# Kernel tuning notes

Measured on AMD Instinct MI355X. Metric: run time of the kernel, lower is better.

Reference implementation:

```python
import jax, jax.numpy as jnp
import numpy as np

B, S, D = 4, 2048, 1024
H = 4 * D          # expert hidden dim
E_SPEC = 4         # num specific experts
E_SHR = 2          # num shared experts
TOP_K = 2


def setup_inputs() -> dict:
    key = jax.random.key(0)
    ks = jax.random.split(key, 16)
    s = 0.02
    return {
        "x": jax.random.normal(ks[0], (B, S, D), jnp.float32),
        # specific experts (stacked over expert axis)
        "spec_w1": jax.random.normal(ks[1], (E_SPEC, D, H), jnp.float32) * s,
        "spec_b1": jnp.zeros((E_SPEC, H), jnp.float32),
        "spec_w2": jax.random.normal(ks[2], (E_SPEC, H, D), jnp.float32) * s,
        "spec_b2": jnp.zeros((E_SPEC, D), jnp.float32),
        "spec_rw": jax.random.normal(ks[3], (D, E_SPEC), jnp.float32) * s,
        "spec_rb": jnp.zeros((E_SPEC,), jnp.float32),
        # shared experts
        "shr_w1": jax.random.normal(ks[4], (E_SHR, D, H), jnp.float32) * s,
        "shr_b1": jnp.zeros((E_SHR, H), jnp.float32),
        "shr_w2": jax.random.normal(ks[5], (E_SHR, H, D), jnp.float32) * s,
        "shr_b2": jnp.zeros((E_SHR, D), jnp.float32),
        "shr_rw": jax.random.normal(ks[6], (D, E_SHR), jnp.float32) * s,
        "shr_rb": jnp.zeros((E_SHR,), jnp.float32),
    }


def _expert_mlp(xf, w1, b1, w2, b2):
    # xf: [T, D]; w1: [E, D, H]; w2: [E, H, D] -> [E, T, D]
    h = jax.nn.gelu(jnp.einsum("td,edh->eth", xf, w1) + b1[:, None, :],
                    approximate=False)
    return jnp.einsum("eth,ehd->etd", h, w2) + b2[:, None, :]


def reference(x, spec_w1, spec_b1, spec_w2, spec_b2, spec_rw, spec_rb,
              shr_w1, shr_b1, shr_w2, shr_b2, shr_rw, shr_rb):
    b, s, d = x.shape
    xf = x.reshape(-1, d)                      # [T, D]
    T = xf.shape[0]

    # --- specific (top-k) routing ---
    spec_probs = jax.nn.softmax(xf @ spec_rw + spec_rb, axis=-1)   # [T, E]
    topk_probs, topk_idx = jax.lax.top_k(spec_probs, TOP_K)        # [T, K]

    # aux load-balancing loss
    counts = jnp.zeros((E_SPEC,), jnp.float32).at[topk_idx.reshape(-1)].add(1.0)
    fraction = counts / (T * TOP_K)
    aux_loss = E_SPEC * jnp.sum(fraction * spec_probs.mean(axis=0))

    # gate[t, e] = sum_k topk_probs[t,k] * 1[topk_idx[t,k]==e]
    gate = jnp.sum(jax.nn.one_hot(topk_idx, E_SPEC, dtype=xf.dtype)
                   * topk_probs[..., None], axis=1)                # [T, E]

    spec_out_e = _expert_mlp(xf, spec_w1, spec_b1, spec_w2, spec_b2)  # [E, T, D]
    specific_out = jnp.einsum("te,etd->td", gate, spec_out_e)

    # --- shared (dense) experts ---
    shr_probs = jax.nn.softmax(xf @ shr_rw + shr_rb, axis=-1)      # [T, E_shr]
    shr_out_e = _expert_mlp(xf, shr_w1, shr_b1, shr_w2, shr_b2)    # [E_shr, T, D]
    shared_out = jnp.einsum("te,etd->td", shr_probs, shr_out_e)

    final = (specific_out + shared_out).reshape(b, s, d)
    return final, aux_loss
```

## Files before the change

kernel.cpp:

```cpp
#include <hip/hip_runtime.h>
#include <hip/hip_bf16.h>

#define T_TOK 8192
#define DDIM 1024
#define HDIM 4096

typedef __bf16 bf16;
typedef bf16 bf16x8 __attribute__((ext_vector_type(8)));
typedef float f32x4 __attribute__((ext_vector_type(4)));

#define ASM_VMCNT(n) asm volatile("s_waitcnt vmcnt(" #n ")" ::: "memory")
#define MFMA16(a, b, c) __builtin_amdgcn_mfma_f32_16x16x32_bf16((a), (b), (c), 0, 0, 0)
#define G8_BAR __builtin_amdgcn_s_barrier()
#define G8_WAIT                                            \
  asm volatile("s_waitcnt lgkmcnt(0)" ::: "memory");       \
  __builtin_amdgcn_sched_barrier(0)

__device__ __forceinline__ void gl_lds16(const void* g, void* l) {
  __builtin_amdgcn_global_load_lds(
      (const __attribute__((address_space(1))) unsigned int*)g,
      (__attribute__((address_space(3))) unsigned int*)l, 16, 0, 0);
}

__device__ __forceinline__ float gelu_f(float v) {
  const float x = v * 0.7071067811865475f;
  const float ax = fabsf(x);
  const float t = 1.0f / fmaf(0.3275911f, ax, 1.0f);
  float p = fmaf(1.061405429f, t, -1.453152027f);
  p = fmaf(p, t, 1.421413741f);
  p = fmaf(p, t, -0.284496736f);
  p = fmaf(p, t, 0.254829592f);
  p = p * t;
  const float e = __expf(-ax * ax);
  const float er = fmaf(-p, e, 1.0f);
  const float erfx = (x >= 0.0f) ? er : -er;
  return 0.5f * v * (1.0f + erfx);
}

__global__ __launch_bounds__(256) void conv_router(
    const float* __restrict__ x, bf16* __restrict__ xb,
    const float* __restrict__ srw, const float* __restrict__ srb,
    const float* __restrict__ hrw, const float* __restrict__ hrb,
    float* __restrict__ gate, float4* __restrict__ probs4,
    int* __restrict__ top2) {
  const int lane = threadIdx.x & 63;
  const int w = threadIdx.x >> 6;
  const int t = blockIdx.x * 4 + w;

  const float* xr = x + (size_t)t * DDIM;
  bf16* xbr = xb + (size_t)t * DDIM;
  float p0 = 0, p1 = 0, p2 = 0, p3 = 0, p4 = 0, p5 = 0;
#pragma unroll
  for (int c = 0; c < 4; ++c) {
    const int d = c * 256 + lane * 4;
    const float4 xv = *(const float4*)(xr + d);
    bf16 ov[4] = {(bf16)xv.x, (bf16)xv.y, (bf16)xv.z, (bf16)xv.w};
    *(float2*)(xbr + d) = *(float2*)ov;
    const float xa[4] = {xv.x, xv.y, xv.z, xv.w};
#pragma unroll
    for (int j = 0; j < 4; ++j) {
      const float xd = xa[j];
      const float4 r4 = *(const float4*)(srw + (size_t)(d + j) * 4);
      p0 += xd * r4.x; p1 += xd * r4.y; p2 += xd * r4.z; p3 += xd * r4.w;
      const float2 r2 = *(const float2*)(hrw + (size_t)(d + j) * 2);
      p4 += xd * r2.x; p5 += xd * r2.y;
    }
  }
#pragma unroll
  for (int off = 32; off >= 1; off >>= 1) {
    p0 += __shfl_xor(p0, off);
    p1 += __shfl_xor(p1, off);
    p2 += __shfl_xor(p2, off);
    p3 += __shfl_xor(p3, off);
    p4 += __shfl_xor(p4, off);
    p5 += __shfl_xor(p5, off);
  }
  if (lane == 0) {
    const float l0 = p0 + srb[0], l1 = p1 + srb[1];
    const float l2 = p2 + srb[2], l3 = p3 + srb[3];
    const float m = fmaxf(fmaxf(l0, l1), fmaxf(l2, l3));
    const float e0 = expf(l0 - m), e1 = expf(l1 - m);
    const float e2 = expf(l2 - m), e3 = expf(l3 - m);
    const float s = e0 + e1 + e2 + e3;
    float pr[4] = {e0 / s, e1 / s, e2 / s, e3 / s};
    int i1 = 0; float v1 = pr[0];
#pragma unroll
    for (int e = 1; e < 4; ++e) if (pr[e] > v1) { v1 = pr[e]; i1 = e; }
    int i2 = -1; float v2 = -1.0f;
#pragma unroll
    for (int e = 0; e < 4; ++e)
      if (e != i1 && pr[e] > v2) { v2 = pr[e]; i2 = e; }
    float g[4] = {0, 0, 0, 0};
    g[i1] = v1; g[i2] = v2;
    float* gr = gate + (size_t)t * 8;
    gr[0] = g[0]; gr[1] = g[1]; gr[2] = g[2]; gr[3] = g[3];
    const float h0 = p4 + hrb[0], h1 = p5 + hrb[1];
    const float mh = fmaxf(h0, h1);
    const float q0 = expf(h0 - mh), q1 = expf(h1 - mh);
    const float qs = q0 + q1;
    gr[4] = q0 / qs; gr[5] = q1 / qs; gr[6] = 0; gr[7] = 0;
    probs4[t] = make_float4(pr[0], pr[1], pr[2], pr[3]);
    top2[t] = i1 | (i2 << 8);
  }
}

__global__ __launch_bounds__(256) void transpose_convert6(
    const float* __restrict__ spec_w, const float* __restrict__ shr_w,
    bf16* __restrict__ dst, int R, int C) {
  __shared__ float tile[32][33];
  const int z = blockIdx.z;
  const float* src = (z < 4) ? spec_w + (size_t)z * R * C
                             : shr_w + (size_t)(z - 4) * R * C;
  bf16* d = dst + (size_t)z * R * C;
  const int c0 = blockIdx.x * 32, r0 = blockIdx.y * 32;
  const int tx = threadIdx.x & 31, ty = threadIdx.x >> 5;
#pragma unroll
  for (int i = 0; i < 4; ++i)
    tile[ty + 8 * i][tx] = src[(size_t)(r0 + ty + 8 * i) * C + c0 + tx];
  __syncthreads();
#pragma unroll
  for (int i = 0; i < 4; ++i)
    d[(size_t)(c0 + ty + 8 * i) * R + r0 + tx] = (bf16)tile[tx][ty + 8 * i];
}

__global__ __launch_bounds__(1024) void scan_build(
    const int* __restrict__ top2, const float4* __restrict__ probs4,
    int* __restrict__ meta, int* __restrict__ lists,
    float* __restrict__ auxg) {
  __shared__ unsigned long long sc[1024];
  __shared__ float4 rp[512];
  const int tid = threadIdx.x;

  int ee[8];
  unsigned long long c = 0;
  float4 ps = make_float4(0.f, 0.f, 0.f, 0.f);
#pragma unroll
  for (int j = 0; j < 8; ++j) {
    const int t = tid * 8 + j;
    const int p = top2[t];
    ee[j] = p;
    const int a = p & 15, b = (p >> 8) & 15;
    c += (1ULL << (16 * a)) + (1ULL << (16 * b));
    const float4 pv = probs4[t];
    ps.x += pv.x; ps.y += pv.y; ps.z += pv.z; ps.w += pv.w;
  }
  sc[tid] = c;
  __syncthreads();
  for (int off = 1; off < 1024; off <<= 1) {
    const unsigned long long mine = sc[tid];
    const unsigned long long prev = (tid >= off) ? sc[tid - off] : 0ULL;
    __syncthreads();
    sc[tid] = mine + prev;
    __syncthreads();
  }
  const unsigned long long incl = sc[tid];
  const unsigned long long tot = sc[1023];
  const unsigned long long excl = incl - c;
  int q0 = (int)(excl & 0xffff), q1 = (int)((excl >> 16) & 0xffff);
  int q2 = (int)((excl >> 32) & 0xffff), q3 = (int)((excl >> 48) & 0xffff);
#pragma unroll
  for (int j = 0; j < 8; ++j) {
    const int t = tid * 8 + j;
    const int a = ee[j] & 15, b = (ee[j] >> 8) & 15;
    const int pa = (a == 0) ? q0 : (a == 1) ? q1 : (a == 2) ? q2 : q3;
    lists[a * 8192 + pa] = t;
    q0 += (a == 0); q1 += (a == 1); q2 += (a == 2); q3 += (a == 3);
    const int pb = (b == 0) ? q0 : (b == 1) ? q1 : (b == 2) ? q2 : q3;
    lists[b * 8192 + pb] = t;
    q0 += (b == 0); q1 += (b == 1); q2 += (b == 2); q3 += (b == 3);
  }
  if (tid == 1023) {
    const int c0 = (int)(tot & 0xffff), c1 = (int)((tot >> 16) & 0xffff);
    const int c2 = (int)((tot >> 32) & 0xffff), c3 = (int)((tot >> 48) & 0xffff);
    meta[24] = c0; meta[25] = c1; meta[26] = c2; meta[27] = c3;
    auxg[0] = (float)c0; auxg[1] = (float)c1;
    auxg[2] = (float)c2; auxg[3] = (float)c3;
    const int nb0 = (c0 + 255) >> 8, nb1 = (c1 + 255) >> 8;
    const int nb2 = (c2 + 255) >> 8, nb3 = (c3 + 255) >> 8;
    const int ch0 = (nb0 + 3) >> 2, ch1 = (nb1 + 3) >> 2;
    const int ch2 = (nb2 + 3) >> 2, ch3 = (nb3 + 3) >> 2;
    meta[34] = 0;
    meta[35] = nb0 * 256;
    meta[36] = meta[35] + nb1 * 256;
    meta[37] = meta[36] + nb2 * 256;
    meta[40] = 0;
    meta[41] = 64 * ch0;
    meta[42] = meta[41] + 64 * ch1;
    meta[43] = meta[42] + 64 * ch2;
    meta[44] = meta[43] + 64 * ch3;
  }
  if (tid >= 512) rp[tid - 512] = ps;
  __syncthreads();
  if (tid < 512) {
    const float4 o = rp[tid];
    ps.x += o.x; ps.y += o.y; ps.z += o.z; ps.w += o.w;
  }
  for (int w = 256; w >= 1; w >>= 1) {
    __syncthreads();
    if (tid >= w && tid < 2 * w) rp[tid - w] = ps;
    __syncthreads();
    if (tid < w) {
      const float4 o = rp[tid];
      ps.x += o.x; ps.y += o.y; ps.z += o.z; ps.w += o.w;
    }
  }
  if (tid == 0) {
    auxg[4] = ps.x; auxg[5] = ps.y; auxg[6] = ps.z; auxg[7] = ps.w;
  }
}

__global__ void aux_finalize(const float* __restrict__ auxg,
                             float* __restrict__ outp) {
  float a = 0.0f;
#pragma unroll
  for (int e = 0; e < 4; ++e)
    a += (auxg[e] / (float)(T_TOK * 2)) * (auxg[4 + e] / (float)T_TOK);
  outp[0] = 4.0f * a;
}

template <int KIND>
__global__ __launch_bounds__(512, 2) void g8(
    const bf16* __restrict__ A, const bf16* __restrict__ Bw,
    const float* __restrict__ bias, bf16* __restrict__ h_all, int N,
    int CH_M, int CH_N, const int* __restrict__ meta,
    const int* __restrict__ lists, int e) {
  __shared__ __align__(1024) bf16 Alds[2 * 256 * 64];
  __shared__ __align__(1024) bf16 Blds[2 * 256 * 64];

  const int tid = threadIdx.x;
  const int lane = tid & 63, wid = tid >> 6;
  const int wm = wid >> 2, wn = wid & 3;
  const int lr = lane & 15, lg = lane >> 4;

  int bm, bn, hb = 0, s = e;
  const bf16* Bp = Bw;
  const float* biasp = bias;
  if constexpr (KIND == 0) {
    const int xcd = blockIdx.x & 7, idx = blockIdx.x >> 3;
    bm = (xcd >> 1) * CH_M + idx / CH_N;
    bn = (xcd & 1) * CH_N + idx % CH_N;
  } else if constexpr (KIND == 1) {
    const int b = blockIdx.x;
    if (b >= meta[44]) return;
    s = (b >= meta[41]) + (b >= meta[42]) + (b >= meta[43]);
    const int local = b - meta[40 + s];
    const int nbm = (meta[24 + s] + 255) >> 8;
    const int CHm = (nbm + 3) >> 2;
    if (local >= 64 * CHm) return;
    const int xc = local & 7, idx = local >> 3;
    bm = (xc >> 1) * CHm + idx / 8;
    bn = (xc & 1) * 8 + idx % 8;
    if (bm >= nbm) return;
    hb = meta[34 + s];
    Bp = Bw + (size_t)s * DDIM * HDIM;
    biasp = bias + (size_t)s * HDIM;
  } else {
    const int nbm = (meta[24 + e] + 255) >> 8;
    const int CHm = (nbm + 3) >> 2;
    if (blockIdx.x >= 64 * CHm) return;
    const int xc = blockIdx.x & 7, idx = blockIdx.x >> 3;
    bm = (xc >> 1) * CHm + idx / 8;
    bn = (xc & 1) * 8 + idx % 8;
    if (bm >= nbm) return;
  }
  const int K = DDIM;
  const int NT = K >> 6;

  const int rl = tid >> 3;
  const int cbs = ((tid * 16) & 127) ^ ((rl & 7) << 4);
  int ar[4];
#pragma unroll
  for (int c = 0; c < 4; ++c) ar[c] = bm * 256 + c * 64 + rl;
  if constexpr (KIND != 0) {
    const int* lp = lists + s * 8192;
#pragma unroll
    for (int c = 0; c < 4; ++c) {
      const int t = lp[ar[c]];
      ar[c] = t < 0 ? 0 : t;
    }
  }
  const bf16* sA[4];
  const bf16* sB[4];
#pragma unroll
  for (int c = 0; c < 4; ++c) {
    sA[c] = A + (size_t)ar[c] * K + (cbs >> 1);
    sB[c] = Bp + (size_t)(bn * 256 + c * 64 + rl) * K + (cbs >> 1);
  }
  char* const ldsA = (char*)Alds;
  char* const ldsB = (char*)Blds;
  const int wb = wid * 1024;

  const int ax0 = (lg * 16) ^ ((lr & 7) << 4);
  const int ax1 = ax0 ^ 64;
  const int aro = (wm * 128 + lr) * 128;
  const int bro = (wn * 64 + lr) * 128;
  const char* const A0 = (const char*)Alds + aro + ax0;
  const char* const A1 = (const char*)Alds + aro + ax1;
  const char* const B0 = (const char*)Blds + bro + ax0;
  const char* const B1 = (const char*)Blds + bro + ax1;

  f32x4 acc[8][4] = {};
  bf16x8 af[4][2], b01[2][2], b23[2][2];

#define G8_RA(BOFF, MB)                                               \
  _Pragma("unroll") for (int i = 0; i < 4; ++i) {                     \
    af[i][0] = *(const bf16x8*)(A0 + (BOFF) + ((MB) + i) * 2048);     \
    af[i][1] = *(const bf16x8*)(A1 + (BOFF) + ((MB) + i) * 2048);     \
  }
#define G8_RB(BOFF, DST, NB)                                          \
  _Pragma("unroll") for (int i = 0; i < 2; ++i) {                     \
    DST[i][0] = *(const bf16x8*)(B0 + (BOFF) + ((NB) + i) * 2048);    \
    DST[i][1] = *(const bf16x8*)(B1 + (BOFF) + ((NB) + i) * 2048);    \
  }
#define G8_MMA(MB, NB, BSRC)                                          \
  __builtin_amdgcn_s_setprio(1);                                      \
  _Pragma("unroll") for (int i = 0; i < 4; ++i)                       \
    _Pragma("unroll") for (int j = 0; j < 2; ++j) {                   \
      acc[(MB) + i][(NB) + j] =                                       \
          MFMA16(af[i][0], BSRC[j][0], acc[(MB) + i][(NB) + j]);      \
      acc[(MB) + i][(NB) + j] =                                       \
          MFMA16(af[i][1], BSRC[j][1], acc[(MB) + i][(NB) + j]);      \
    }                                                                 \
  __builtin_amdgcn_s_setprio(0);
#define G8_STG_B(T, C, BUFO)                                          \
  gl_lds16(sB[C] + (size_t)(T) * 64, ldsB + (BUFO) + (C) * 8192 + wb);
#define G8_STG_A(T, C, BUFO)                                          \
  gl_lds16(sA[C] + (size_t)(T) * 64, ldsA + (BUFO) + (C) * 8192 + wb);

  G8_STG_B(0, 0, 0) G8_STG_B(0, 1, 0) G8_STG_B(0, 2, 0) G8_STG_B(0, 3, 0)
  G8_STG_A(0, 0, 0) G8_STG_A(0, 1, 0) G8_STG_A(0, 2, 0) G8_STG_A(0, 3, 0)
  G8_STG_B(1, 0, 32768) G8_STG_B(1, 1, 32768)
  G8_STG_B(1, 2, 32768) G8_STG_B(1, 3, 32768)
  G8_STG_A(1, 0, 32768) G8_STG_A(1, 1, 32768)
  G8_STG_A(1, 2, 32768) G8_STG_A(1, 3, 32768)
  ASM_VMCNT(8);
  G8_BAR;

  for (int t = 0; t < NT; t += 2) {
    const bool stg = (t + 2) < NT;
    G8_RA(0, 0);
    G8_RB(0, b01, 0);
    G8_BAR; G8_WAIT;
    G8_MMA(0, 0, b01);
    G8_BAR;
    G8_RB(0, b23, 2);
    G8_BAR; G8_WAIT;
    G8_MMA(0, 2, b23);
    G8_BAR;
    G8_RA(0, 4);
    if (stg) { G8_STG_B(t + 2, 0, 0) G8_STG_B(t + 2, 1, 0) }
    G8_BAR; G8_WAIT;
    G8_MMA(4, 0, b01);
    G8_BAR;
    if (stg) { G8_STG_B(t + 2, 2, 0) G8_STG_B(t + 2, 3, 0) }
    G8_MMA(4, 2, b23);
    if (stg) ASM_VMCNT(4); else ASM_VMCNT(0);
    G8_BAR;
    G8_RA(32768, 0);
    G8_RB(32768, b01, 0);
    if (stg) { G8_STG_A(t + 2, 0, 0) G8_STG_A(t + 2, 1, 0) }
    G8_BAR; G8_WAIT;
    G8_MMA(0, 0, b01);
    G8_BAR;
    G8_RB(32768, b23, 2);
    if (stg) { G8_STG_A(t + 2, 2, 0) G8_STG_A(t + 2, 3, 0) }
    G8_BAR; G8_WAIT;
    G8_MMA(0, 2, b23);
    G8_BAR;
    G8_RA(32768, 4);
    if (stg) {
      G8_STG_B(t + 3, 0, 32768) G8_STG_B(t + 3, 1, 32768)
      G8_STG_B(t + 3, 2, 32768) G8_STG_B(t + 3, 3, 32768)
    }
    G8_BAR; G8_WAIT;
    G8_MMA(4, 0, b01);
    G8_BAR;
    if (stg) {
      G8_STG_A(t + 3, 0, 32768) G8_STG_A(t + 3, 1, 32768)
      G8_STG_A(t + 3, 2, 32768) G8_STG_A(t + 3, 3, 32768)
    }
    G8_MMA(4, 2, b23);
    if (stg) ASM_VMCNT(8);
    G8_BAR;
  }

  const int colb = bn * 256 + wn * 64;
  const int rowb = hb + bm * 256 + wm * 128 + lg * 4;
  float bv[4];
#pragma unroll
  for (int nf = 0; nf < 4; ++nf) bv[nf] = biasp[colb + nf * 16 + lr];
#pragma unroll
  for (int mf = 0; mf < 8; ++mf)
#pragma unroll
    for (int nf = 0; nf < 4; ++nf) {
      const int col = colb + nf * 16 + lr;
#pragma unroll
      for (int r = 0; r < 4; ++r) {
        const int row = rowb + mf * 16 + r;
        h_all[(size_t)row * N + col] = (bf16)gelu_f(acc[mf][nf][r] + bv[nf]);
      }
    }
}

template <int EMODE>
__global__ __launch_bounds__(512, 2) void g2k(
    const bf16* __restrict__ A, int lda, const bf16* __restrict__ B,
    const float* __restrict__ bias, float* __restrict__ out,
    const float* __restrict__ gate, int gidx, const int* __restrict__ meta,
    const int* __restrict__ lists, int e, int packed) {
  __shared__ __align__(1024) bf16 Alds[2 * 256 * 64];
  __shared__ __align__(1024) bf16 Blds[2 * 128 * 64];

  const int tid = threadIdx.x;
  const int lane = tid & 63, wid = tid >> 6;
  const int wm = wid >> 2, wn = wid & 3;
  const int lr = lane & 15, lg = lane >> 4;

  int bm, bn, hb = 0;
  if constexpr (EMODE == 3) {
    const int nbm = (meta[24 + e] + 255) >> 8;
    const int CHm = (nbm + 3) >> 2;
    if (blockIdx.x >= 8 * CHm * 4) return;
    const int xc = blockIdx.x & 7, idx = blockIdx.x >> 3;
    bm = (xc >> 1) * CHm + idx / 4;
    bn = (xc & 1) * 4 + idx % 4;
    if (bm >= nbm) return;
    hb = packed ? meta[34 + e] : 0;
  } else {
    const int xcd = blockIdx.x & 7, idx = blockIdx.x >> 3;
    bm = (xcd >> 1) * 8 + idx / 4;
    bn = (xcd & 1) * 4 + idx % 4;
  }
  const int K = HDIM, N = DDIM;
  const int NT = K >> 6;

  const int L = tid * 16;
  const int rl = L >> 7;
  const int colb = (L & 127) ^ ((rl & 7) << 4);

  const int ar0 = hb + bm * 256 + rl;
  const bf16* sAc0 = A + (size_t)ar0 * lda + (colb >> 1);
  const bf16* sAc1 = A + (size_t)(ar0 + 64) * lda + (colb >> 1);
  const bf16* sAc2 = A + (size_t)(ar0 + 128) * lda + (colb >> 1);
  const bf16* sAc3 = A + (size_t)(ar0 + 192) * lda + (colb >> 1);
  const bf16* sB = B + (size_t)(bn * 128 + rl) * K + (colb >> 1);

  char* const ldsA = (char*)Alds;
  char* const ldsB = (char*)Blds;
  const int wb = wid * 1024;
  char* const stA[2] = {ldsA + wb, ldsA + 32768 + wb};
  char* const stB[2] = {ldsB + wb, ldsB + 16384 + wb};

  const int ax0 = (lg * 16) ^ ((lr & 7) << 4);
  const int ax1 = ax0 ^ 64;
  const int aro = (wm * 128 + lr) * 128;
  const int bro = (wn * 32 + lr) * 128;
  const char* const Ak0[2] = {ldsA + aro + ax0, ldsA + 32768 + aro + ax0};
  const char* const Ak1[2] = {ldsA + aro + ax1, ldsA + 32768 + aro + ax1};
  const char* const Bk0[2] = {ldsB + bro + ax0, ldsB + 16384 + bro + ax0};
  const char* const Bk1[2] = {ldsB + bro + ax1, ldsB + 16384 + bro + ax1};

  f32x4 acc[8][2] = {};

  gl_lds16(sAc0, stA[0]);
  gl_lds16(sAc1, stA[0] + 8192);
  gl_lds16(sAc2, stA[0] + 16384);
  gl_lds16(sAc3, stA[0] + 24576);
  gl_lds16(sB, stB[0]);
  gl_lds16(sB + (size_t)64 * K, stB[0] + 8192);
  gl_lds16(sB + 64, stB[1]);
  gl_lds16(sB + (size_t)64 * K + 64, stB[1] + 8192);
  gl_lds16(sAc0 + 64, stA[1]);
  gl_lds16(sAc1 + 64, stA[1] + 8192);
  ASM_VMCNT(4);
  __builtin_amdgcn_s_barrier();

  for (int kt0 = 0; kt0 < NT; kt0 += 2) {
#pragma unroll
    for (int par = 0; par < 2; ++par) {
      const int kt = kt0 + par;
      const int cur = par, oth = par ^ 1;
      const bool st1 = (kt + 1) < NT, st2 = (kt + 2) < NT;
      const size_t ko1 = (size_t)(kt + 1) << 6, ko2 = (size_t)(kt + 2) << 6;
      const char* Ac0 = Ak0[cur]; const char* Ac1 = Ak1[cur];
      const char* Bc0 = Bk0[cur]; const char* Bc1 = Bk1[cur];

      bf16x8 af[4][2], bfr[2][2];

#pragma unroll
      for (int mf = 0; mf < 4; ++mf) {
        af[mf][0] = *(const bf16x8*)(Ac0 + mf * 2048);
        af[mf][1] = *(const bf16x8*)(Ac1 + mf * 2048);
      }
      bfr[0][0] = *(const bf16x8*)(Bc0);
      bfr[0][1] = *(const bf16x8*)(Bc1);
      if (st1) {
        gl_lds16(sAc2 + ko1, stA[oth] + 16384);
        gl_lds16(sAc3 + ko1, stA[oth] + 24576);
      }
      __builtin_amdgcn_s_barrier();
      asm volatile("s_waitcnt lgkmcnt(0)" ::: "memory");
      __builtin_amdgcn_sched_barrier(0);
      __builtin_amdgcn_s_setprio(1);
#pragma unroll
      for (int mf = 0; mf < 4; ++mf) {
        acc[mf][0] = MFMA16(af[mf][0], bfr[0][0], acc[mf][0]);
        acc[mf][0] = MFMA16(af[mf][1], bfr[0][1], acc[mf][0]);
      }
      __builtin_amdgcn_s_setprio(0);
      __builtin_amdgcn_s_barrier();

      bfr[1][0] = *(const bf16x8*)(Bc0 + 2048);
      bfr[1][1] = *(const bf16x8*)(Bc1 + 2048);
      __builtin_amdgcn_s_barrier();
      asm volatile("s_waitcnt lgkmcnt(0)" ::: "memory");
      __builtin_amdgcn_sched_barrier(0);
      __builtin_amdgcn_s_setprio(1);
#pragma unroll
      for (int mf = 0; mf < 4; ++mf) {
        acc[mf][1] = MFMA16(af[mf][0], bfr[1][0], acc[mf][1]);
        acc[mf][1] = MFMA16(af[mf][1], bfr[1][1], acc[mf][1]);
      }
      __builtin_amdgcn_s_setprio(0);
      __builtin_amdgcn_s_barrier();

#pragma unroll
      for (int mf = 0; mf < 4; ++mf) {
        af[mf][0] = *(const bf16x8*)(Ac0 + 8192 + mf * 2048);
        af[mf][1] = *(const bf16x8*)(Ac1 + 8192 + mf * 2048);
      }
      if (st2) {
        gl_lds16(sB + ko2, stB[cur]);
        gl_lds16(sB + (size_t)64 * K + ko2, stB[cur] + 8192);
      }
      __builtin_amdgcn_s_barrier();
      asm volatile("s_waitcnt lgkmcnt(0)" ::: "memory");
      __builtin_amdgcn_sched_barrier(0);
      __builtin_amdgcn_s_setprio(1);
#pragma unroll
      for (int mf = 0; mf < 4; ++mf) {
        acc[4 + mf][0] = MFMA16(af[mf][0], bfr[0][0], acc[4 + mf][0]);
        acc[4 + mf][0] = MFMA16(af[mf][1], bfr[0][1], acc[4 + mf][0]);
      }
      __builtin_amdgcn_s_setprio(0);
      __builtin_amdgcn_s_barrier();

      if (st2) {
        gl_lds16(sAc0 + ko2, stA[cur]);
        gl_lds16(sAc1 + ko2, stA[cur] + 8192);
      }
      __builtin_amdgcn_s_setprio(1);
#pragma unroll
      for (int mf = 0; mf < 4; ++mf) {
        acc[4 + mf][1] = MFMA16(af[mf][0], bfr[1][0], acc[4 + mf][1]);
        acc[4 + mf][1] = MFMA16(af[mf][1], bfr[1][1], acc[4 + mf][1]);
      }
      __builtin_amdgcn_s_setprio(0);
      if (st2) {
        ASM_VMCNT(4);
        __builtin_amdgcn_s_barrier();
      } else if (st1) {
        ASM_VMCNT(0);
        __builtin_amdgcn_s_barrier();
      }
    }
  }

  const int colb2 = bn * 128 + wn * 32;
  const int rowb = bm * 256 + wm * 128 + lg * 4;
  float bv[2];
#pragma unroll
  for (int nf = 0; nf < 2; ++nf) bv[nf] = bias[colb2 + nf * 16 + lr];
#pragma unroll
  for (int mf = 0; mf < 8; ++mf) {
    if constexpr (EMODE != 3) {
      float gv[4];
#pragma unroll
      for (int r = 0; r < 4; ++r)
        gv[r] = gate[(size_t)(rowb + mf * 16 + r) * 8 + gidx];
#pragma unroll
      for (int nf = 0; nf < 2; ++nf) {
        const int col = colb2 + nf * 16 + lr;
#pragma unroll
        for (int r = 0; r < 4; ++r) {
          const float v = acc[mf][nf][r] + bv[nf];
          const size_t oi = (size_t)(rowb + mf * 16 + r) * N + col;
          if constexpr (EMODE == 1)
            out[oi] += gv[r] * v;
          else
            out[oi] = gv[r] * v;
        }
      }
    } else {
      const int* lp = lists + e * 8192;
      int tok[4]; float gv[4];
#pragma unroll
      for (int r = 0; r < 4; ++r) {
        tok[r] = lp[rowb + mf * 16 + r];
        gv[r] = tok[r] >= 0 ? gate[(size_t)tok[r] * 8 + gidx] : 0.0f;
      }
#pragma unroll
      for (int nf = 0; nf < 2; ++nf) {
        const int col = colb2 + nf * 16 + lr;
#pragma unroll
        for (int r = 0; r < 4; ++r) {
          if (tok[r] >= 0) {
            const float v = acc[mf][nf][r] + bv[nf];
            out[(size_t)tok[r] * N + col] += gv[r] * v;
          }
        }
      }
    }
  }
}

extern "C" void kernel_launch(void* const* d_in, const int* in_sizes, int n_in,
                              void* d_out, int out_size, void* d_ws,
                              size_t ws_size, hipStream_t stream) {
  const float* x = (const float*)d_in[0];
  const float* spec_w1 = (const float*)d_in[1];
  const float* spec_b1 = (const float*)d_in[2];
  const float* spec_w2 = (const float*)d_in[3];
  const float* spec_b2 = (const float*)d_in[4];
  const float* spec_rw = (const float*)d_in[5];
  const float* spec_rb = (const float*)d_in[6];
  const float* shr_w1 = (const float*)d_in[7];
  const float* shr_b1 = (const float*)d_in[8];
  const float* shr_w2 = (const float*)d_in[9];
  const float* shr_b2 = (const float*)d_in[10];
  const float* shr_rw = (const float*)d_in[11];
  const float* shr_rb = (const float*)d_in[12];
  float* out = (float*)d_out;

  char* ws = (char*)d_ws;
  const size_t DH = (size_t)DDIM * HDIM;
  const size_t OFF_W1 = 16777216;
  const size_t OFF_W2 = OFF_W1 + 50331648;
  const size_t OFF_GATE = OFF_W2 + 50331648;
  const size_t OFF_AUX = OFF_GATE + 262144;
  const size_t OFF_META = OFF_AUX + 256;
  const size_t OFF_LIST = OFF_META + 256;
  const size_t OFF_T2 = OFF_LIST + 131072;
  const size_t OFF_P4 = OFF_T2 + 32768;
  const size_t OFF_H = OFF_P4 + 131072 + 1024;
  bf16* xb = (bf16*)ws;
  bf16* w1t = (bf16*)(ws + OFF_W1);
  bf16* w2t = (bf16*)(ws + OFF_W2);
  float* gate = (float*)(ws + OFF_GATE);
  float* auxg = (float*)(ws + OFF_AUX);
  int* meta = (int*)(ws + OFF_META);
  int* lists = (int*)(ws + OFF_LIST);
  int* top2 = (int*)(ws + OFF_T2);
  float4* probs4 = (float4*)(ws + OFF_P4);
  bf16* h = (bf16*)(ws + OFF_H);

  const bool rich = ws_size >= OFF_H + (size_t)17408 * HDIM * 2;

  hipMemsetAsync(lists, 0xFF, 4 * 8192 * 4, stream);

  conv_router<<<T_TOK / 4, 256, 0, stream>>>(x, xb, spec_rw, spec_rb, shr_rw,
                                             shr_rb, gate, probs4, top2);
  scan_build<<<1, 1024, 0, stream>>>(top2, probs4, meta, lists, auxg);

  transpose_convert6<<<dim3(HDIM / 32, DDIM / 32, 6), 256, 0, stream>>>(
      spec_w1, shr_w1, w1t, DDIM, HDIM);
  transpose_convert6<<<dim3(DDIM / 32, HDIM / 32, 6), 256, 0, stream>>>(
      spec_w2, shr_w2, w2t, HDIM, DDIM);

  if (rich) {
    g8<0><<<1024, 512, 0, stream>>>(xb, w1t + 4 * DH, shr_b1, h, 8192,
                                    8, 16, meta, lists, 0);
    g2k<0><<<256, 512, 0, stream>>>(h, 8192, w2t + 4 * DH, shr_b2, out,
                                    gate, 4, meta, lists, 0, 0);
    g2k<1><<<256, 512, 0, stream>>>(h + 4096, 8192, w2t + 5 * DH,
                                    shr_b2 + 1024, out, gate, 5, meta,
                                    lists, 0, 0);
    g8<1><<<2048, 512, 0, stream>>>(xb, w1t, spec_b1, h, 4096,
                                    0, 8, meta, lists, 0);
    for (int e = 0; e < 4; ++e)
      g2k<3><<<256, 512, 0, stream>>>(h, 4096, w2t + (size_t)e * DH,
                                      spec_b2 + (size_t)e * DDIM, out, gate,
                                      e, meta, lists, e, 1);
  } else {
    for (int es = 0; es < 2; ++es) {
      g8<0><<<512, 512, 0, stream>>>(xb, w1t + (4 + es) * DH,
                                     shr_b1 + (size_t)es * HDIM, h, 4096,
                                     8, 8, meta, lists, 0);
      if (es == 0)
        g2k<0><<<256, 512, 0, stream>>>(h, 4096, w2t + 4 * DH, shr_b2, out,
                                        gate, 4, meta, lists, 0, 0);
      else
        g2k<1><<<256, 512, 0, stream>>>(h, 4096, w2t + 5 * DH,
                                        shr_b2 + 1024, out, gate, 5, meta,
                                        lists, 0, 0);
    }
    for (int e = 0; e < 4; ++e) {
      g8<2><<<512, 512, 0, stream>>>(xb, w1t + (size_t)e * DH,
                                     spec_b1 + (size_t)e * HDIM, h, 4096,
                                     0, 8, meta, lists, e);
      g2k<3><<<256, 512, 0, stream>>>(h, 4096, w2t + (size_t)e * DH,
                                      spec_b2 + (size_t)e * DDIM, out, gate,
                                      e, meta, lists, e, 0);
    }
  }
  aux_finalize<<<1, 1, 0, stream>>>(auxg, out + (size_t)T_TOK * DDIM);
}
```

Before: 1.016 ms.

## Batch specific-expert down-projection into one grouped GEMM with gather reduce

Replaces the four per-expert down-projection launches, which scattered gated results into the output with read-modify-write, with a single grouped GEMM over all experts' packed hidden rows. That GEMM writes gated bf16 partials into a scratch buffer that reuses the w1 workspace. A new per-token reduce kernel then gathers each token's two partials via recorded list positions and adds them to the output. This removes the scattered atomic-free RMW traffic and the extra launches, at the cost of a bf16 intermediate round trip and reduced precision of the partials. It also drops the fallback path for small workspaces.

```diff
diff --git a/kernel.cpp b/kernel.cpp
--- a/kernel.cpp
+++ b/kernel.cpp
@@ -125,7 +125,7 @@
 
 __global__ __launch_bounds__(1024) void scan_build(
     const int* __restrict__ top2, const float4* __restrict__ probs4,
-    int* __restrict__ meta, int* __restrict__ lists,
+    int* __restrict__ meta, int* __restrict__ lists, int2* __restrict__ tpos,
     float* __restrict__ auxg) {
   __shared__ unsigned long long sc[1024];
   __shared__ float4 rp[512];
@@ -168,6 +168,7 @@
     const int pb = (b == 0) ? q0 : (b == 1) ? q1 : (b == 2) ? q2 : q3;
     lists[b * 8192 + pb] = t;
     q0 += (b == 0); q1 += (b == 1); q2 += (b == 2); q3 += (b == 3);
+    tpos[t] = make_int2(a * 8192 + pa, b * 8192 + pb);
   }
   if (tid == 1023) {
     const int c0 = (int)(tot & 0xffff), c1 = (int)((tot >> 16) & 0xffff);
@@ -188,6 +189,11 @@
     meta[42] = meta[41] + 64 * ch1;
     meta[43] = meta[42] + 64 * ch2;
     meta[44] = meta[43] + 64 * ch3;
+    meta[52] = 0;
+    meta[53] = 16 * ch0;
+    meta[54] = meta[53] + 16 * ch1;
+    meta[55] = meta[54] + 16 * ch2;
+    meta[56] = meta[55] + 16 * ch3;
   }
   if (tid >= 512) rp[tid - 512] = ps;
   __syncthreads();
@@ -221,9 +227,9 @@
 template <int KIND>
 __global__ __launch_bounds__(512, 2) void g8(
     const bf16* __restrict__ A, const bf16* __restrict__ Bw,
-    const float* __restrict__ bias, bf16* __restrict__ h_all, int N,
+    const float* __restrict__ bias, bf16* __restrict__ Out, int N,
     int CH_M, int CH_N, const int* __restrict__ meta,
-    const int* __restrict__ lists, int e) {
+    const int* __restrict__ lists, const float* __restrict__ gate) {
   __shared__ __align__(1024) bf16 Alds[2 * 256 * 64];
   __shared__ __align__(1024) bf16 Blds[2 * 256 * 64];
 
@@ -232,7 +238,7 @@
   const int wm = wid >> 2, wn = wid & 3;
   const int lr = lane & 15, lg = lane >> 4;
 
-  int bm, bn, hb = 0, s = e;
+  int bm, bn, hb = 0, s = 0;
   const bf16* Bp = Bw;
   const float* biasp = bias;
   if constexpr (KIND == 0) {
@@ -255,29 +261,39 @@
     Bp = Bw + (size_t)s * DDIM * HDIM;
     biasp = bias + (size_t)s * HDIM;
   } else {
-    const int nbm = (meta[24 + e] + 255) >> 8;
+    const int b = blockIdx.x;
+    if (b >= meta[56]) return;
+    s = (b >= meta[53]) + (b >= meta[54]) + (b >= meta[55]);
+    const int local = b - meta[52 + s];
+    const int nbm = (meta[24 + s] + 255) >> 8;
     const int CHm = (nbm + 3) >> 2;
-    if (blockIdx.x >= 64 * CHm) return;
-    const int xc = blockIdx.x & 7, idx = blockIdx.x >> 3;
-    bm = (xc >> 1) * CHm + idx / 8;
-    bn = (xc & 1) * 8 + idx % 8;
+    if (local >= 16 * CHm) return;
+    const int xc = local & 7, idx = local >> 3;
+    bm = (xc >> 1) * CHm + idx / 2;
+    bn = (xc & 1) * 2 + idx % 2;
     if (bm >= nbm) return;
-  }
-  const int K = DDIM;
-  const int NT = K >> 6;
+    hb = meta[34 + s];
+    Bp = Bw + (size_t)s * DDIM * HDIM;
+    biasp = bias + (size_t)s * DDIM;
+  }
+  constexpr int K = (KIND == 2) ? HDIM : DDIM;
+  constexpr int NT = K >> 6;
 
   const int rl = tid >> 3;
   const int cbs = ((tid * 16) & 127) ^ ((rl & 7) << 4);
   int ar[4];
 #pragma unroll
   for (int c = 0; c < 4; ++c) ar[c] = bm * 256 + c * 64 + rl;
-  if constexpr (KIND != 0) {
+  if constexpr (KIND == 1) {
     const int* lp = lists + s * 8192;
 #pragma unroll
     for (int c = 0; c < 4; ++c) {
       const int t = lp[ar[c]];
       ar[c] = t < 0 ? 0 : t;
     }
+  } else if constexpr (KIND == 2) {
+#pragma unroll
+    for (int c = 0; c < 4; ++c) ar[c] += hb;
   }
   const bf16* sA[4];
   const bf16* sB[4];
@@ -385,29 +401,53 @@
   }
 
   const int colb = bn * 256 + wn * 64;
-  const int rowb = hb + bm * 256 + wm * 128 + lg * 4;
-  float bv[4];
-#pragma unroll
-  for (int nf = 0; nf < 4; ++nf) bv[nf] = biasp[colb + nf * 16 + lr];
-#pragma unroll
-  for (int mf = 0; mf < 8; ++mf)
-#pragma unroll
-    for (int nf = 0; nf < 4; ++nf) {
-      const int col = colb + nf * 16 + lr;
+  const int lrowb = bm * 256 + wm * 128 + lg * 4;
+  if constexpr (KIND != 2) {
+    float bv[4];
+#pragma unroll
+    for (int nf = 0; nf < 4; ++nf) bv[nf] = biasp[colb + nf * 16 + lr];
+#pragma unroll
+    for (int mf = 0; mf < 8; ++mf)
+#pragma unroll
+      for (int nf = 0; nf < 4; ++nf) {
+        const int col = colb + nf * 16 + lr;
+#pragma unroll
+        for (int r = 0; r < 4; ++r) {
+          const int row = hb + lrowb + mf * 16 + r;
+          Out[(size_t)row * N + col] = (bf16)gelu_f(acc[mf][nf][r] + bv[nf]);
+        }
+      }
+  } else {
+    float bv[4];
+#pragma unroll
+    for (int nf = 0; nf < 4; ++nf) bv[nf] = biasp[colb + nf * 16 + lr];
+    const int* lp = lists + s * 8192;
+#pragma unroll
+    for (int mf = 0; mf < 8; ++mf) {
+      int tok[4]; float gv[4];
 #pragma unroll
       for (int r = 0; r < 4; ++r) {
-        const int row = rowb + mf * 16 + r;
-        h_all[(size_t)row * N + col] = (bf16)gelu_f(acc[mf][nf][r] + bv[nf]);
+        tok[r] = lp[lrowb + mf * 16 + r];
+        gv[r] = tok[r] >= 0 ? gate[(size_t)tok[r] * 8 + s] : 0.0f;
+      }
+#pragma unroll
+      for (int nf = 0; nf < 4; ++nf) {
+        const int col = colb + nf * 16 + lr;
+#pragma unroll
+        for (int r = 0; r < 4; ++r) {
+          const float v = gv[r] * (acc[mf][nf][r] + bv[nf]);
+          Out[(size_t)(hb + lrowb + mf * 16 + r) * N + col] = (bf16)v;
+        }
       }
     }
+  }
 }
 
 template <int EMODE>
 __global__ __launch_bounds__(512, 2) void g2k(
     const bf16* __restrict__ A, int lda, const bf16* __restrict__ B,
     const float* __restrict__ bias, float* __restrict__ out,
-    const float* __restrict__ gate, int gidx, const int* __restrict__ meta,
-    const int* __restrict__ lists, int e, int packed) {
+    const float* __restrict__ gate, int gidx) {
   __shared__ __align__(1024) bf16 Alds[2 * 256 * 64];
   __shared__ __align__(1024) bf16 Blds[2 * 128 * 64];
 
@@ -416,21 +456,9 @@
   const int wm = wid >> 2, wn = wid & 3;
   const int lr = lane & 15, lg = lane >> 4;
 
-  int bm, bn, hb = 0;
-  if constexpr (EMODE == 3) {
-    const int nbm = (meta[24 + e] + 255) >> 8;
-    const int CHm = (nbm + 3) >> 2;
-    if (blockIdx.x >= 8 * CHm * 4) return;
-    const int xc = blockIdx.x & 7, idx = blockIdx.x >> 3;
-    bm = (xc >> 1) * CHm + idx / 4;
-    bn = (xc & 1) * 4 + idx % 4;
-    if (bm >= nbm) return;
-    hb = packed ? meta[34 + e] : 0;
-  } else {
-    const int xcd = blockIdx.x & 7, idx = blockIdx.x >> 3;
-    bm = (xcd >> 1) * 8 + idx / 4;
-    bn = (xcd & 1) * 4 + idx % 4;
-  }
+  const int xcd = blockIdx.x & 7, idx = blockIdx.x >> 3;
+  const int bm = (xcd >> 1) * 8 + idx / 4;
+  const int bn = (xcd & 1) * 4 + idx % 4;
   const int K = HDIM, N = DDIM;
   const int NT = K >> 6;
 
@@ -438,7 +466,7 @@
   const int rl = L >> 7;
   const int colb = (L & 127) ^ ((rl & 7) << 4);
 
-  const int ar0 = hb + bm * 256 + rl;
+  const int ar0 = bm * 256 + rl;
   const bf16* sAc0 = A + (size_t)ar0 * lda + (colb >> 1);
   const bf16* sAc1 = A + (size_t)(ar0 + 64) * lda + (colb >> 1);
   const bf16* sAc2 = A + (size_t)(ar0 + 128) * lda + (colb >> 1);
@@ -573,45 +601,42 @@
   for (int nf = 0; nf < 2; ++nf) bv[nf] = bias[colb2 + nf * 16 + lr];
 #pragma unroll
   for (int mf = 0; mf < 8; ++mf) {
-    if constexpr (EMODE != 3) {
-      float gv[4];
-#pragma unroll
-      for (int r = 0; r < 4; ++r)
-        gv[r] = gate[(size_t)(rowb + mf * 16 + r) * 8 + gidx];
-#pragma unroll
-      for (int nf = 0; nf < 2; ++nf) {
-        const int col = colb2 + nf * 16 + lr;
-#pragma unroll
-        for (int r = 0; r < 4; ++r) {
-          const float v = acc[mf][nf][r] + bv[nf];
-          const size_t oi = (size_t)(rowb + mf * 16 + r) * N + col;
-          if constexpr (EMODE == 1)
-            out[oi] += gv[r] * v;
-          else
-            out[oi] = gv[r] * v;
-        }
-      }
-    } else {
-      const int* lp = lists + e * 8192;
-      int tok[4]; float gv[4];
+    float gv[4];
+#pragma unroll
+    for (int r = 0; r < 4; ++r)
+      gv[r] = gate[(size_t)(rowb + mf * 16 + r) * 8 + gidx];
+#pragma unroll
+    for (int nf = 0; nf < 2; ++nf) {
+      const int col = colb2 + nf * 16 + lr;
 #pragma unroll
       for (int r = 0; r < 4; ++r) {
-        tok[r] = lp[rowb + mf * 16 + r];
-        gv[r] = tok[r] >= 0 ? gate[(size_t)tok[r] * 8 + gidx] : 0.0f;
-      }
-#pragma unroll
-      for (int nf = 0; nf < 2; ++nf) {
-        const int col = colb2 + nf * 16 + lr;
-#pragma unroll
-        for (int r = 0; r < 4; ++r) {
-          if (tok[r] >= 0) {
-            const float v = acc[mf][nf][r] + bv[nf];
-            out[(size_t)tok[r] * N + col] += gv[r] * v;
-          }
-        }
+        const float v = acc[mf][nf][r] + bv[nf];
+        const size_t oi = (size_t)(rowb + mf * 16 + r) * N + col;
+        if constexpr (EMODE == 1)
+          out[oi] += gv[r] * v;
+        else
+          out[oi] = gv[r] * v;
       }
     }
   }
+}
+
+__global__ __launch_bounds__(256) void reduce_spec(
+    const bf16* __restrict__ P, const int2* __restrict__ tpos,
+    const int* __restrict__ meta, float* __restrict__ out) {
+  const int t = blockIdx.x;
+  const int c = threadIdx.x * 4;
+  const int2 tp = tpos[t];
+  const int ea = tp.x >> 13, pa = tp.x & 8191;
+  const int eb = tp.y >> 13, pb = tp.y & 8191;
+  const bf16* A4 = &P[(size_t)(meta[34 + ea] + pa) * DDIM + c];
+  const bf16* B4 = &P[(size_t)(meta[34 + eb] + pb) * DDIM + c];
+  float4 o = *(float4*)&out[(size_t)t * DDIM + c];
+  o.x += (float)A4[0] + (float)B4[0];
+  o.y += (float)A4[1] + (float)B4[1];
+  o.z += (float)A4[2] + (float)B4[2];
+  o.w += (float)A4[3] + (float)B4[3];
+  *(float4*)&out[(size_t)t * DDIM + c] = o;
 }
 
 extern "C" void kernel_launch(void* const* d_in, const int* in_sizes, int n_in,
@@ -642,7 +667,8 @@
   const size_t OFF_LIST = OFF_META + 256;
   const size_t OFF_T2 = OFF_LIST + 131072;
   const size_t OFF_P4 = OFF_T2 + 32768;
-  const size_t OFF_H = OFF_P4 + 131072 + 1024;
+  const size_t OFF_TPOS = OFF_P4 + 131072 + 1024;
+  const size_t OFF_H = OFF_TPOS + 65536;
   bf16* xb = (bf16*)ws;
   bf16* w1t = (bf16*)(ws + OFF_W1);
   bf16* w2t = (bf16*)(ws + OFF_W2);
@@ -652,56 +678,32 @@
   int* lists = (int*)(ws + OFF_LIST);
   int* top2 = (int*)(ws + OFF_T2);
   float4* probs4 = (float4*)(ws + OFF_P4);
+  int2* tpos = (int2*)(ws + OFF_TPOS);
   bf16* h = (bf16*)(ws + OFF_H);
-
-  const bool rich = ws_size >= OFF_H + (size_t)17408 * HDIM * 2;
+  bf16* P = w1t;
 
   hipMemsetAsync(lists, 0xFF, 4 * 8192 * 4, stream);
 
   conv_router<<<T_TOK / 4, 256, 0, stream>>>(x, xb, spec_rw, spec_rb, shr_rw,
                                              shr_rb, gate, probs4, top2);
-  scan_build<<<1, 1024, 0, stream>>>(top2, probs4, meta, lists, auxg);
+  scan_build<<<1, 1024, 0, stream>>>(top2, probs4, meta, lists, tpos, auxg);
 
   transpose_convert6<<<dim3(HDIM / 32, DDIM / 32, 6), 256, 0, stream>>>(
       spec_w1, shr_w1, w1t, DDIM, HDIM);
   transpose_convert6<<<dim3(DDIM / 32, HDIM / 32, 6), 256, 0, stream>>>(
       spec_w2, shr_w2, w2t, HDIM, DDIM);
 
-  if (rich) {
-    g8<0><<<1024, 512, 0, stream>>>(xb, w1t + 4 * DH, shr_b1, h, 8192,
-                                    8, 16, meta, lists, 0);
-    g2k<0><<<256, 512, 0, stream>>>(h, 8192, w2t + 4 * DH, shr_b2, out,
-                                    gate, 4, meta, lists, 0, 0);
-    g2k<1><<<256, 512, 0, stream>>>(h + 4096, 8192, w2t + 5 * DH,
-                                    shr_b2 + 1024, out, gate, 5, meta,
-                                    lists, 0, 0);
-    g8<1><<<2048, 512, 0, stream>>>(xb, w1t, spec_b1, h, 4096,
-                                    0, 8, meta, lists, 0);
-    for (int e = 0; e < 4; ++e)
-      g2k<3><<<256, 512, 0, stream>>>(h, 4096, w2t + (size_t)e * DH,
-                                      spec_b2 + (size_t)e * DDIM, out, gate,
-                                      e, meta, lists, e, 1);
-  } else {
-    for (int es = 0; es < 2; ++es) {
-      g8<0><<<512, 512, 0, stream>>>(xb, w1t + (4 + es) * DH,
-                                     shr_b1 + (size_t)es * HDIM, h, 4096,
-                                     8, 8, meta, lists, 0);
-      if (es == 0)
-        g2k<0><<<256, 512, 0, stream>>>(h, 4096, w2t + 4 * DH, shr_b2, out,
-                                        gate, 4, meta, lists, 0, 0);
-      else
-        g2k<1><<<256, 512, 0, stream>>>(h, 4096, w2t + 5 * DH,
-                                        shr_b2 + 1024, out, gate, 5, meta,
-                                        lists, 0, 0);
-    }
-    for (int e = 0; e < 4; ++e) {
-      g8<2><<<512, 512, 0, stream>>>(xb, w1t + (size_t)e * DH,
-                                     spec_b1 + (size_t)e * HDIM, h, 4096,
-                                     0, 8, meta, lists, e);
-      g2k<3><<<256, 512, 0, stream>>>(h, 4096, w2t + (size_t)e * DH,
-                                      spec_b2 + (size_t)e * DDIM, out, gate,
-                                      e, meta, lists, e, 0);
-    }
-  }
+  g8<0><<<1024, 512, 0, stream>>>(xb, w1t + 4 * DH, shr_b1, h, 8192,
+                                  8, 16, meta, lists, nullptr);
+  g2k<0><<<256, 512, 0, stream>>>(h, 8192, w2t + 4 * DH, shr_b2, out,
+                                  gate, 4);
+  g2k<1><<<256, 512, 0, stream>>>(h + 4096, 8192, w2t + 5 * DH,
+                                  shr_b2 + 1024, out, gate, 5);
+  g8<1><<<2048, 512, 0, stream>>>(xb, w1t, spec_b1, h, 4096,
+                                  0, 8, meta, lists, nullptr);
+  g8<2><<<512, 512, 0, stream>>>(h, w2t, spec_b2, P, DDIM,
+                                 0, 2, meta, lists, gate);
+  reduce_spec<<<T_TOK, 256, 0, stream>>>(P, tpos, meta, out);
+
   aux_finalize<<<1, 1, 0, stream>>>(auxg, out + (size_t)T_TOK * DDIM);
 }
```

Result: faster. 890.7 us (-12.3%).
